# Performance work log

Measured on AMD Instinct MI355X. Metric: run time of the kernel, lower is better.

## Reference

```python
import jax, jax.numpy as jnp
import numpy as np

B, S, D_MODEL = 2, 2048, 768
N_QK, D_QK = 16, 16
N_OV, D_OV = 256, 1
VKV = 16
ROT_DIM, ROT_BASE = 16, 10000.0
SCALE = D_QK ** 0.5  # attn_scale defaults to sqrt(d_qk_head)


def _rotary_sin_cos(n_ctx, rotary_dim, base):
    # TransformerLens-style, non-adjacent pairs (GPT-NeoX)
    pos = jnp.arange(n_ctx, dtype=jnp.float32)
    dim = jnp.arange(rotary_dim // 2, dtype=jnp.float32)
    freq = base ** (dim / (rotary_dim / 2))
    freq = jnp.concatenate([freq, freq])  # 'd -> (2 d)'
    angles = pos[:, None] / freq[None, :]  # [n_ctx, rotary_dim]
    return jnp.sin(angles), jnp.cos(angles)


def _apply_rotary(x, sin, cos):
    # x: [B, S, H, d_head]; rotate first ROT_DIM dims, pass through the rest
    s = x.shape[1]
    xr = x[..., :ROT_DIM]
    half = ROT_DIM // 2
    rot = jnp.concatenate([-xr[..., half:], xr[..., :half]], axis=-1)  # rotate_every_two (non-adjacent)
    xr = xr * cos[:s, None, :] + rot * sin[:s, None, :]
    return jnp.concatenate([xr, x[..., ROT_DIM:]], axis=-1) if x.shape[-1] > ROT_DIM else xr


def setup_inputs() -> dict:
    key = jax.random.key(0)
    ks = jax.random.split(key, 6)
    std_qk = np.sqrt(2.0 / (D_MODEL * D_QK))   # kaiming fan_in for [H, d_model, d_head]
    std_v = np.sqrt(2.0 / (D_MODEL * D_OV))
    std_o = np.sqrt(2.0 / (D_OV * D_MODEL))
    std_vk = np.sqrt(2.0 / (N_QK * D_QK))
    return {
        "resid": jax.random.normal(ks[0], (B, S, D_MODEL), jnp.float32),
        "W_Q": jax.random.normal(ks[1], (N_QK, D_MODEL, D_QK), jnp.float32) * std_qk,
        "W_K": jax.random.normal(ks[2], (N_QK, D_MODEL, D_QK), jnp.float32) * std_qk,
        "W_V": jax.random.normal(ks[3], (N_OV, D_MODEL, D_OV), jnp.float32) * std_v,
        "W_O": jax.random.normal(ks[4], (N_OV, D_OV, D_MODEL), jnp.float32) * std_o,
        "b_Q": jnp.zeros((N_QK, D_QK), jnp.float32),
        "b_K": jnp.zeros((N_QK, D_QK), jnp.float32),
        "b_V": jnp.zeros((N_OV, D_OV), jnp.float32),
        "b_O": jnp.zeros((D_MODEL,), jnp.float32),
        "virtual_k": jax.random.normal(ks[5], (VKV, N_QK, D_QK), jnp.float32) * std_vk,
        "virtual_v": jnp.zeros((VKV, N_OV, D_OV), jnp.float32),
    }


def reference(resid, W_Q, W_K, W_V, W_O, b_Q, b_K, b_V, b_O, virtual_k, virtual_v):
    b, s, _ = resid.shape
    sin, cos = _rotary_sin_cos(s, ROT_DIM, ROT_BASE)

    q = jnp.einsum('bsd,hde->bshe', resid, W_Q) + b_Q  # [B,S,N_QK,D_QK]
    k = jnp.einsum('bsd,hde->bshe', resid, W_K) + b_K
    v = jnp.einsum('bsd,hde->bshe', resid, W_V) + b_V  # [B,S,N_OV,1]

    q = _apply_rotary(q, sin, cos)
    k = _apply_rotary(k, sin, cos)

    # append virtual KV along key axis
    k = jnp.concatenate([k, jnp.broadcast_to(virtual_k[None], (b, VKV, N_QK, D_QK))], axis=1)
    v = jnp.concatenate([v, jnp.broadcast_to(virtual_v[None], (b, VKV, N_OV, D_OV))], axis=1)

    scores = jnp.einsum('bqhe,bkhe->bhqk', q, k) / SCALE  # [B,H,S,S+VKV]
    i = jnp.arange(s)[:, None]
    j = jnp.arange(s + VKV)[None, :]
    mask = (j - i) <= VKV  # tril(.., diagonal=VKV)
    scores = jnp.where(mask, scores, -jnp.inf)
    pattern = jax.nn.softmax(scores, axis=-1)
    pattern = jnp.where(jnp.isnan(pattern), 0.0, pattern)

    r = N_OV // N_QK
    v_r = v.transpose(0, 2, 1, 3).reshape(b, N_QK, r, s + VKV, D_OV)  # [B,n_qk,r,K,1]
    z = jnp.einsum('bnqk,bnrkh->bnrqh', pattern, v_r)  # [B,n_qk,r,S,1]
    z = z.reshape(b, N_OV, s, D_OV).transpose(0, 2, 1, 3)  # [B,S,N_OV,1]

    out = jnp.einsum('bqhd,hdm->bqm', z, W_O) + b_O  # [B,S,D_MODEL]
    return out
```

## Files before the change

### kernel.cpp

```cpp
#include <hip/hip_runtime.h>
#include <hip/hip_bf16.h>
#include <math.h>

#define B_   2
#define S_   2048
#define DM   768
#define H_   16
#define C_   256
#define VKV_ 16
#define SK   2064
#define SKP  2080
#define NT_  65

#define TSPLIT 16
#define MAXSP  5
#define NACT   164

typedef __attribute__((ext_vector_type(8))) short short8;
typedef __attribute__((ext_vector_type(4))) short short4v;
typedef __attribute__((ext_vector_type(4))) float f32x4;
typedef __attribute__((ext_vector_type(16))) float f32x16;
typedef __attribute__((ext_vector_type(4))) unsigned uint4v;

#define QSCALE 0.360673760222240851f
#define L2B8   1.6609640474436811f

__device__ __forceinline__ short tobf(float f) {
    union { float f; unsigned u; } x; x.f = f;
    unsigned r = x.u + 0x7FFFu + ((x.u >> 16) & 1u);
    return (short)(r >> 16);
}
__device__ __forceinline__ float frombf_lo(unsigned u) {
    union { unsigned u; float f; } x; x.u = u << 16; return x.f;
}
__device__ __forceinline__ float frombf_hi(unsigned u) {
    union { unsigned u; float f; } x; x.u = u & 0xFFFF0000u; return x.f;
}

__device__ __forceinline__ void gload_lds16(const short* g, short* l) {
    __builtin_amdgcn_global_load_lds(
        (const __attribute__((address_space(1))) unsigned int*)g,
        (__attribute__((address_space(3))) unsigned int*)l, 16, 0, 0);
}

#define NRES (4096*768/4)
#define NWQ  (768*768)
#define NWO  (768*256)
__global__ __launch_bounds__(256) void conv_all(
    const float* __restrict__ resid,
    const float* __restrict__ WQ, const float* __restrict__ WK,
    const float* __restrict__ WV, const float* __restrict__ WO,
    const float* __restrict__ bQ, const float* __restrict__ bK,
    const float* __restrict__ bV,
    const float* __restrict__ vKp, const float* __restrict__ vVp,
    short* __restrict__ Ab, short* __restrict__ Wqkv_t,
    short* __restrict__ WtO, float* __restrict__ bqkv,
    short* __restrict__ Kb2, short* __restrict__ Vt3)
{
    int t = blockIdx.x * 256 + threadIdx.x;
    if (t < NRES) {
        float4 v = *(const float4*)(resid + (size_t)t * 4);
        short4v o = { tobf(v.x), tobf(v.y), tobf(v.z), tobf(v.w) };
        *(short4v*)(Ab + (size_t)t * 4) = o;
        return;
    }
    t -= NRES;
    if (t < NWQ) {
        int cc, d;
        if (t < 512 * 768) {
            const int e    = t & 15;
            const int rest = t >> 4;
            d  = rest % 768;
            cc = (rest / 768) * 16 + e;
        } else { cc = t / 768; d = t % 768; }
        float w;
        if (cc < 256)      w = WQ[((size_t)(cc >> 4) * DM + d) * 16 + (cc & 15)];
        else if (cc < 512) w = WK[((size_t)((cc - 256) >> 4) * DM + d) * 16 + (cc & 15)];
        else               w = WV[(size_t)(cc - 512) * DM + d];
        Wqkv_t[(size_t)cc * 768 + d] = tobf(w);
        return;
    }
    t -= NWQ;
    if (t < NWO) {
        int c = t & 255, m = t >> 8;
        WtO[t] = tobf(WO[(size_t)c * DM + m]);
        return;
    }
    t -= NWO;
    if (t < 768) {
        bqkv[t] = (t < 256) ? bQ[t] : (t < 512 ? bK[t - 256] : bV[t - 512]);
        return;
    }
    t -= 768;
    if (t < 32 * 32) {
        const int bh = t >> 5;
        const int s  = S_ + (t & 31);
        const int h  = bh & 15;
        short kb[16], vb[16];
        if (s < SK) {
            const int tt = s - S_;
#pragma unroll
            for (int e = 0; e < 16; ++e) {
                kb[e] = tobf(vKp[(size_t)tt * 256 + h * 16 + e]);
                vb[e] = tobf(vVp[(size_t)tt * 256 + h * 16 + e]);
            }
        } else {
#pragma unroll
            for (int e = 0; e < 16; ++e) { kb[e] = 0; vb[e] = 0; }
        }
        const int t5 = s >> 5;
        short* kbase = Kb2 + ((size_t)bh * NT_ + t5) * 512 + (s & 31) * 8;
#pragma unroll
        for (int e = 0; e < 8; ++e)  { kbase[e] = kb[e]; kbase[256 + e] = kb[e + 8]; }
        short* vbase = Vt3 + ((size_t)bh * NT_ + t5) * 1024
                     + ((s >> 4) & 1) * 512 + ((s >> 3) & 1) * 8 + (s & 7);
#pragma unroll
        for (int dv = 0; dv < 16; ++dv) vbase[dv * 16] = vb[dv];
    }
}

__global__ __launch_bounds__(256) void mm_qkv(
    const short* __restrict__ A, const short* __restrict__ Bt,
    const float* __restrict__ bias,
    short* __restrict__ Qb2, short* __restrict__ Kb2, short* __restrict__ Vt3)
{
    __shared__ float CtS[64][65];
    short* As = (short*)&CtS[0][0];
    short* Bs = As + 4096;

    const int tid  = threadIdx.x;
    const int w    = tid >> 6;
    const int lane = tid & 63;
    const int wm   = w >> 1, wn = w & 1;
    const int g    = lane >> 4, c = lane & 15;

    const int linear = blockIdx.y * 12 + blockIdx.x;
    const int xcd  = linear & 7;
    const int jj2  = linear >> 3;
    const int m0   = (xcd * 8 + jj2 / 12) * 64;
    const int n0   = (jj2 % 12) * 64;

    f32x4 acc[2][2];
#pragma unroll
    for (int i = 0; i < 2; ++i)
#pragma unroll
        for (int j = 0; j < 2; ++j) acc[i][j] = (f32x4){0.f, 0.f, 0.f, 0.f};

    const int lr = lane >> 3;
    const int lc = lane & 7;

    for (int k0 = 0; k0 < 768; k0 += 64) {
#pragma unroll
        for (int i = 0; i < 2; ++i) {
            const int ch  = i * 4 + w;
            const int row = ch * 8 + lr;
            const int scc = lc ^ (row & 7);
            gload_lds16(A + (size_t)(m0 + row) * 768 + k0 + scc * 8, As + ch * 512);
        }
#pragma unroll
        for (int i = 0; i < 2; ++i) {
            const int ch  = i * 4 + w;
            const int row = ch * 8 + lr;
            const int scc = lc ^ (row & 7);
            gload_lds16(Bt + (size_t)(n0 + row) * 768 + k0 + scc * 8, Bs + ch * 512);
        }
        __syncthreads();
#pragma unroll
        for (int kk = 0; kk < 64; kk += 32) {
            short8 af[2], bf[2];
#pragma unroll
            for (int i = 0; i < 2; ++i) {
                const int row = wm * 32 + i * 16 + c;
                const int sc  = ((kk >> 3) + g) ^ (row & 7);
                af[i] = *(const short8*)(As + row * 64 + sc * 8);
            }
#pragma unroll
            for (int j = 0; j < 2; ++j) {
                const int row = wn * 32 + j * 16 + c;
                const int sc  = ((kk >> 3) + g) ^ (row & 7);
                bf[j] = *(const short8*)(Bs + row * 64 + sc * 8);
            }
#pragma unroll
            for (int i = 0; i < 2; ++i)
#pragma unroll
                for (int j = 0; j < 2; ++j)
                    acc[i][j] = __builtin_amdgcn_mfma_f32_16x16x32_bf16(
                        af[i], bf[j], acc[i][j], 0, 0, 0);
        }
        __syncthreads();
    }

#pragma unroll
    for (int i = 0; i < 2; ++i)
#pragma unroll
        for (int j = 0; j < 2; ++j)
#pragma unroll
            for (int r = 0; r < 4; ++r)
                CtS[wm * 32 + i * 16 + 4 * g + r][wn * 32 + j * 16 + c] = acc[i][j][r];
    __syncthreads();

    const int b = m0 >> 11;
    if (n0 < 512) {
        const int isQ   = n0 < 256;
        const int hbase = (n0 & 255) >> 4;
        const int srow = tid & 63;
        const int g16  = tid >> 6;
        const int s    = (m0 + srow) & 2047;
        const int bh   = b * 16 + hbase + g16;
        float v[16];
#pragma unroll
        for (int e = 0; e < 16; ++e)
            v[e] = CtS[srow][g16 * 16 + e] + bias[n0 + g16 * 16 + e];
        union { short s[16]; short8 v8[2]; } u;
#pragma unroll
        for (int e = 0; e < 8; ++e) {
            const float invf = __builtin_amdgcn_exp2f(-(float)e * L2B8);
            float sn, cs;
            __sincosf((float)s * invf, &sn, &cs);
            float o0 = v[e] * cs - v[e + 8] * sn;
            float o1 = v[e + 8] * cs + v[e] * sn;
            if (isQ) { o0 *= QSCALE; o1 *= QSCALE; }
            u.s[e] = tobf(o0); u.s[e + 8] = tobf(o1);
        }
        short* dst = (isQ ? Qb2 + ((size_t)bh * 64 + (s >> 5)) * 512
                          : Kb2 + ((size_t)bh * NT_ + (s >> 5)) * 512)
                   + (s & 31) * 8;
        *(short8*)dst         = u.v8[0];
        *(short8*)(dst + 256) = u.v8[1];
    } else {
        const int hbase = (n0 - 512) >> 4;
        const int dvl = tid & 63;
        const int rg  = tid >> 6;
        const int s0  = (m0 + rg * 16) & 2047;
        const int bh  = b * 16 + hbase + (dvl >> 4);
        const float bv = bias[n0 + dvl];
        union { short s[16]; short8 v8[2]; } u;
#pragma unroll
        for (int k = 0; k < 16; ++k)
            u.s[k] = tobf(CtS[rg * 16 + k][dvl] + bv);
        short* dst = Vt3 + ((size_t)bh * NT_ + (s0 >> 5)) * 1024
                   + ((s0 >> 4) & 1) * 512 + (dvl & 15) * 16;
        *(short8*)dst       = u.v8[0];
        *(short8*)(dst + 8) = u.v8[1];
    }
}

__global__ __launch_bounds__(256) void mm_out(
    const short* __restrict__ A, const short* __restrict__ Bt,
    const float* __restrict__ bias, float* __restrict__ Cout)
{
    __shared__ short As[4096];
    __shared__ short Bs[4096];

    const int tid  = threadIdx.x;
    const int w    = tid >> 6;
    const int lane = tid & 63;
    const int wm   = w >> 1, wn = w & 1;
    const int g    = lane >> 4, c = lane & 15;

    const int linear = blockIdx.y * 12 + blockIdx.x;
    const int xcd  = linear & 7;
    const int jj2  = linear >> 3;
    const int m0   = (xcd * 8 + jj2 / 12) * 64;
    const int n0   = (jj2 % 12) * 64;

    f32x4 acc[2][2];
#pragma unroll
    for (int i = 0; i < 2; ++i)
#pragma unroll
        for (int j = 0; j < 2; ++j) acc[i][j] = (f32x4){0.f, 0.f, 0.f, 0.f};

    const int lr = lane >> 3;
    const int lc = lane & 7;

    for (int k0 = 0; k0 < 256; k0 += 64) {
#pragma unroll
        for (int i = 0; i < 2; ++i) {
            const int ch  = i * 4 + w;
            const int row = ch * 8 + lr;
            const int scc = lc ^ (row & 7);
            gload_lds16(A + (size_t)(m0 + row) * 256 + k0 + scc * 8, As + ch * 512);
        }
#pragma unroll
        for (int i = 0; i < 2; ++i) {
            const int ch  = i * 4 + w;
            const int row = ch * 8 + lr;
            const int scc = lc ^ (row & 7);
            gload_lds16(Bt + (size_t)(n0 + row) * 256 + k0 + scc * 8, Bs + ch * 512);
        }
        __syncthreads();
#pragma unroll
        for (int kk = 0; kk < 64; kk += 32) {
            short8 af[2], bf[2];
#pragma unroll
            for (int i = 0; i < 2; ++i) {
                const int row = wm * 32 + i * 16 + c;
                const int sc  = ((kk >> 3) + g) ^ (row & 7);
                af[i] = *(const short8*)(As + row * 64 + sc * 8);
            }
#pragma unroll
            for (int j = 0; j < 2; ++j) {
                const int row = wn * 32 + j * 16 + c;
                const int sc  = ((kk >> 3) + g) ^ (row & 7);
                bf[j] = *(const short8*)(Bs + row * 64 + sc * 8);
            }
#pragma unroll
            for (int i = 0; i < 2; ++i)
#pragma unroll
                for (int j = 0; j < 2; ++j)
                    acc[i][j] = __builtin_amdgcn_mfma_f32_16x16x32_bf16(
                        af[i], bf[j], acc[i][j], 0, 0, 0);
        }
        __syncthreads();
    }
#pragma unroll
    for (int i = 0; i < 2; ++i)
#pragma unroll
        for (int j = 0; j < 2; ++j) {
            const int col = n0 + wn * 32 + j * 16 + c;
            const float bv = bias[col];
#pragma unroll
            for (int r = 0; r < 4; ++r) {
                const int row = m0 + wm * 32 + i * 16 + 4 * g + r;
                Cout[(size_t)row * DM + col] = acc[i][j][r] + bv;
            }
        }
}

__global__ __launch_bounds__(256) void attn_split(
    const short* __restrict__ Qb2, const short* __restrict__ Kb2,
    const short* __restrict__ Vt3, unsigned* __restrict__ PartA,
    float* __restrict__ PartL, short* __restrict__ Zb)
{
    const int w    = threadIdx.x >> 6;
    const int lane = threadIdx.x & 63;
    const int blk  = blockIdx.x;
    const int xcd  = blk & 7;
    const int j    = blk >> 3;
    const int bhl  = j / 41;
    const int slot = j - bhl * 41;
    const int bh   = xcd * 4 + bhl;
    const int r    = slot * 4 + w;
    int qt, sp;
    if (r < 49)       { sp = 1; qt = 15 + r; }
    else if (r < 82)  { sp = 2; qt = 31 + (r - 49); }
    else if (r < 99)  { sp = 3; qt = 47 + (r - 82); }
    else if (r == 99) { sp = 4; qt = 63; }
    else              { sp = 0; qt = 163 - r; }

    const int nt   = qt + 2;
    const int t0   = sp * TSPLIT;
    const int tend = min(t0 + TSPLIT, nt);

    const int hi = lane >> 5;
    const int qc = lane & 31;
    const int q0 = qt * 32;

    const f32x16 zero16 = {0,0,0,0,0,0,0,0,0,0,0,0,0,0,0,0};

    short8 qf = *(const short8*)(Qb2 + ((size_t)bh * 64 + qt) * 512 + lane * 8);

    f32x16 acc = zero16;
    float lsum = 0.f;

    const short* kbase = Kb2 + (size_t)bh * NT_ * 512 + lane * 8;
    const short* vbase = Vt3 + (size_t)bh * NT_ * 1024 + (lane & 15) * 16 + hi * 8;
    const int qv16  = q0 + qc + 16;
    const int tmask = (q0 + 17) >> 5;

#define LK(tt)  (*(const short8*)(kbase + (size_t)(tt) * 512))
#define LVA(tt) (*(const short8*)(vbase + (size_t)(tt) * 1024))
#define LVB(tt) (*(const short8*)(vbase + (size_t)(tt) * 1024 + 512))

#define SOFTMAX_TILE(S, tt, B1, B2)                                          \
    {                                                                        \
        if ((tt) >= tmask) {                                                 \
            const int kt_ = (tt) * 32;                                       \
            _Pragma("unroll")                                                \
            for (int rr = 0; rr < 16; ++rr) {                                \
                const int key = kt_ + (rr & 3) + 8 * (rr >> 2) + 4 * hi;     \
                S[rr] = (key <= qv16) ? S[rr] : -INFINITY;                   \
            }                                                                \
        }                                                                    \
        unsigned pk[8];                                                      \
        _Pragma("unroll")                                                    \
        for (int jj = 0; jj < 8; ++jj) {                                     \
            const float p0 = __builtin_amdgcn_exp2f(S[2 * jj]);              \
            const float p1 = __builtin_amdgcn_exp2f(S[2 * jj + 1]);          \
            lsum += p0 + p1;                                                 \
            asm("v_cvt_pk_bf16_f32 %0, %1, %2" : "=v"(pk[jj]) : "v"(p0), "v"(p1)); \
        }                                                                    \
        unsigned a0 = pk[0], a2 = pk[2], a1 = pk[1], a3 = pk[3];             \
        unsigned a4 = pk[4], a6 = pk[6], a5 = pk[5], a7 = pk[7];             \
        asm("v_permlane32_swap_b32 %0, %1" : "+v"(a0), "+v"(a2));            \
        asm("v_permlane32_swap_b32 %0, %1" : "+v"(a1), "+v"(a3));            \
        asm("v_permlane32_swap_b32 %0, %1" : "+v"(a4), "+v"(a6));            \
        asm("v_permlane32_swap_b32 %0, %1" : "+v"(a5), "+v"(a7));            \
        B1.u[0] = a0; B1.u[1] = a1; B1.u[2] = a2; B1.u[3] = a3;              \
        B2.u[0] = a4; B2.u[1] = a5; B2.u[2] = a6; B2.u[3] = a7;              \
    }

    const int npair_end = t0 + ((tend - t0) & ~1);

    if (t0 < npair_end) {
        short8 kfA = LK(t0),     vaA = LVA(t0),     vvA = LVB(t0);
        short8 kfB = LK(t0 + 1), vaB = LVA(t0 + 1), vvB = LVB(t0 + 1);

        for (int t = t0; t < npair_end; t += 2) {
            short8 kfA_n = kfA, vaA_n = vaA, vvA_n = vvA;
            short8 kfB_n = kfB, vaB_n = vaB, vvB_n = vvB;
            if (t + 2 < npair_end) {
                kfA_n = LK(t + 2); vaA_n = LVA(t + 2); vvA_n = LVB(t + 2);
                kfB_n = LK(t + 3); vaB_n = LVA(t + 3); vvB_n = LVB(t + 3);
            }

            __builtin_amdgcn_s_setprio(1);
            f32x16 S0 = __builtin_amdgcn_mfma_f32_32x32x16_bf16(kfA, qf, zero16, 0, 0, 0);
            f32x16 S1 = __builtin_amdgcn_mfma_f32_32x32x16_bf16(kfB, qf, zero16, 0, 0, 0);
            __builtin_amdgcn_s_setprio(0);

            union { unsigned u[4]; short8 v; } b1A, b2A, b1B, b2B;
            SOFTMAX_TILE(S0, t,     b1A, b2A);
            SOFTMAX_TILE(S1, t + 1, b1B, b2B);

            __builtin_amdgcn_s_setprio(1);
            acc = __builtin_amdgcn_mfma_f32_32x32x16_bf16(vaA, b1A.v, acc, 0, 0, 0);
            acc = __builtin_amdgcn_mfma_f32_32x32x16_bf16(vvA, b2A.v, acc, 0, 0, 0);
            acc = __builtin_amdgcn_mfma_f32_32x32x16_bf16(vaB, b1B.v, acc, 0, 0, 0);
            acc = __builtin_amdgcn_mfma_f32_32x32x16_bf16(vvB, b2B.v, acc, 0, 0, 0);
            __builtin_amdgcn_s_setprio(0);

            kfA = kfA_n; vaA = vaA_n; vvA = vvA_n;
            kfB = kfB_n; vaB = vaB_n; vvB = vvB_n;
        }
    }
    if (npair_end < tend) {
        const int t = npair_end;
        short8 kf = LK(t), va = LVA(t), vv = LVB(t);
        f32x16 S0 = __builtin_amdgcn_mfma_f32_32x32x16_bf16(kf, qf, zero16, 0, 0, 0);
        union { unsigned u[4]; short8 v; } b1, b2;
        SOFTMAX_TILE(S0, t, b1, b2);
        acc = __builtin_amdgcn_mfma_f32_32x32x16_bf16(va, b1.v, acc, 0, 0, 0);
        acc = __builtin_amdgcn_mfma_f32_32x32x16_bf16(vv, b2.v, acc, 0, 0, 0);
    }

    lsum += __shfl_xor(lsum, 32);

    if (sp == 0 && qt <= 14) {
        const float inv = 1.f / lsum;
        const int b = bh >> 4, h = bh & 15;
        short* zp = Zb + ((size_t)(b * S_ + q0 + qc)) * C_ + h * 16;
        unsigned o01, o23, o45, o67;
        float a0 = acc[0] * inv, a1 = acc[1] * inv, a2 = acc[2] * inv, a3 = acc[3] * inv;
        float a4 = acc[4] * inv, a5 = acc[5] * inv, a6 = acc[6] * inv, a7 = acc[7] * inv;
        asm("v_cvt_pk_bf16_f32 %0, %1, %2" : "=v"(o01) : "v"(a0), "v"(a1));
        asm("v_cvt_pk_bf16_f32 %0, %1, %2" : "=v"(o23) : "v"(a2), "v"(a3));
        asm("v_cvt_pk_bf16_f32 %0, %1, %2" : "=v"(o45) : "v"(a4), "v"(a5));
        asm("v_cvt_pk_bf16_f32 %0, %1, %2" : "=v"(o67) : "v"(a6), "v"(a7));
        *(unsigned*)(zp + 4 * hi)         = o01;
        *(unsigned*)(zp + 4 * hi + 2)     = o23;
        *(unsigned*)(zp + 8 + 4 * hi)     = o45;
        *(unsigned*)(zp + 8 + 4 * hi + 2) = o67;
        return;
    }

    uint4v pa;
    asm("v_cvt_pk_bf16_f32 %0, %1, %2" : "=v"(pa.x) : "v"(acc[0]), "v"(acc[1]));
    asm("v_cvt_pk_bf16_f32 %0, %1, %2" : "=v"(pa.y) : "v"(acc[2]), "v"(acc[3]));
    asm("v_cvt_pk_bf16_f32 %0, %1, %2" : "=v"(pa.z) : "v"(acc[4]), "v"(acc[5]));
    asm("v_cvt_pk_bf16_f32 %0, %1, %2" : "=v"(pa.w) : "v"(acc[6]), "v"(acc[7]));

    const int pidx = (bh * 64 + qt) * MAXSP + sp;
    *(uint4v*)(PartA + ((size_t)pidx * 64 + lane) * 4) = pa;
    if (hi == 0) PartL[(size_t)pidx * 32 + qc] = lsum;
}

__global__ __launch_bounds__(256) void attn_combine(
    const unsigned* __restrict__ PartA, const float* __restrict__ PartL,
    short* __restrict__ Zb)
{
    const int w    = threadIdx.x >> 6;
    const int lane = threadIdx.x & 63;
    const int wid  = blockIdx.x * 4 + w;
    const int bh   = wid / 49;
    const int qt   = 15 + (wid - bh * 49);
    const int hi   = lane >> 5;
    const int qc   = lane & 31;
    const int ns   = (qt + 2 + TSPLIT - 1) / TSPLIT;

    float a[8];
#pragma unroll
    for (int rr = 0; rr < 8; ++rr) a[rr] = 0.f;
    float lsum = 0.f;

    const int pbase = (bh * 64 + qt) * MAXSP;
    for (int sp = 0; sp < ns; ++sp) {
        uint4v pa = *(const uint4v*)(PartA + ((size_t)(pbase + sp) * 64 + lane) * 4);
        a[0] += frombf_lo(pa.x); a[1] += frombf_hi(pa.x);
        a[2] += frombf_lo(pa.y); a[3] += frombf_hi(pa.y);
        a[4] += frombf_lo(pa.z); a[5] += frombf_hi(pa.z);
        a[6] += frombf_lo(pa.w); a[7] += frombf_hi(pa.w);
        lsum += PartL[(size_t)(pbase + sp) * 32 + qc];
    }
    const float inv = 1.f / lsum;

    const int b = bh >> 4, h = bh & 15;
    const int q0 = qt * 32;
    short* zp = Zb + ((size_t)(b * S_ + q0 + qc)) * C_ + h * 16;
    unsigned o01, o23, o45, o67;
    {
        float a0 = a[0] * inv, a1 = a[1] * inv, a2 = a[2] * inv, a3 = a[3] * inv;
        float a4 = a[4] * inv, a5 = a[5] * inv, a6 = a[6] * inv, a7 = a[7] * inv;
        asm("v_cvt_pk_bf16_f32 %0, %1, %2" : "=v"(o01) : "v"(a0), "v"(a1));
        asm("v_cvt_pk_bf16_f32 %0, %1, %2" : "=v"(o23) : "v"(a2), "v"(a3));
        asm("v_cvt_pk_bf16_f32 %0, %1, %2" : "=v"(o45) : "v"(a4), "v"(a5));
        asm("v_cvt_pk_bf16_f32 %0, %1, %2" : "=v"(o67) : "v"(a6), "v"(a7));
    }
    *(unsigned*)(zp + 4 * hi)         = o01;
    *(unsigned*)(zp + 4 * hi + 2)     = o23;
    *(unsigned*)(zp + 8 + 4 * hi)     = o45;
    *(unsigned*)(zp + 8 + 4 * hi + 2) = o67;
}

extern "C" void kernel_launch(void* const* d_in, const int* in_sizes, int n_in,
                              void* d_out, int out_size, void* d_ws, size_t ws_size,
                              hipStream_t stream)
{
    const float* resid = (const float*)d_in[0];
    const float* WQ = (const float*)d_in[1];
    const float* WK = (const float*)d_in[2];
    const float* WV = (const float*)d_in[3];
    const float* WO = (const float*)d_in[4];
    const float* bQ = (const float*)d_in[5];
    const float* bK = (const float*)d_in[6];
    const float* bV = (const float*)d_in[7];
    const float* bO = (const float*)d_in[8];
    const float* vK = (const float*)d_in[9];
    const float* vV = (const float*)d_in[10];
    float* out = (float*)d_out;
    float* ws  = (float*)d_ws;

    short* Zb   = (short*)ws;
    float* bqkv = ws + 3145728;
    short* Ab   = (short*)(ws + 3145728 + 768);
    short* Wqt  = Ab + 3145728;
    short* WtO  = Wqt + 589824;
    short* Qb2  = WtO + 196608;
    short* Kb2  = Qb2 + 1048576;
    short* Vt3  = Kb2 + 1064960;
    unsigned* PartA = (unsigned*)(Vt3 + 2129920);
    float*    PartL = (float*)(PartA + 2621440);

    const int conv_total = NRES + NWQ + NWO + 768 + 1024;
    conv_all<<<dim3((conv_total + 255) / 256), 256, 0, stream>>>(
        resid, WQ, WK, WV, WO, bQ, bK, bV, vK, vV,
        Ab, Wqt, WtO, bqkv, Kb2, Vt3);
    mm_qkv<<<dim3(12, 64), 256, 0, stream>>>(Ab, Wqt, bqkv, Qb2, Kb2, Vt3);
    attn_split<<<dim3(32 * NACT / 4), 256, 0, stream>>>(Qb2, Kb2, Vt3, PartA, PartL, Zb);
    attn_combine<<<dim3(392), 256, 0, stream>>>(PartA, PartL, Zb);
    mm_out<<<dim3(12, 64), 256, 0, stream>>>(Zb, WtO, bO, out);
}
```

Baseline: 55.47 us.

## Fuse split-K attention combine into one kernel via in-block LDS reduction

Replaces the split attention kernel plus separate combine kernel with one kernel. Each block now owns one (head, query tile) for tiles 15-63, and its four waves each handle a 17-tile slice of keys and reduce their partials through shared memory. Tiles 0-14 are done by one wave each. This drops a kernel launch and the global round-trip of bf16 partials. In exchange, waves with short or empty key ranges sit idle inside a block, load balance changes, and the XCD-aware block mapping is gone.

```diff
diff --git a/kernel.cpp b/kernel.cpp
--- a/kernel.cpp
+++ b/kernel.cpp
@@ -12,15 +12,12 @@
 #define SKP  2080
 #define NT_  65
 
-#define TSPLIT 16
-#define MAXSP  5
-#define NACT   164
+#define TSPLIT 17
 
 typedef __attribute__((ext_vector_type(8))) short short8;
 typedef __attribute__((ext_vector_type(4))) short short4v;
 typedef __attribute__((ext_vector_type(4))) float f32x4;
 typedef __attribute__((ext_vector_type(16))) float f32x16;
-typedef __attribute__((ext_vector_type(4))) unsigned uint4v;
 
 #define QSCALE 0.360673760222240851f
 #define L2B8   1.6609640474436811f
@@ -29,12 +26,6 @@
     union { float f; unsigned u; } x; x.f = f;
     unsigned r = x.u + 0x7FFFu + ((x.u >> 16) & 1u);
     return (short)(r >> 16);
-}
-__device__ __forceinline__ float frombf_lo(unsigned u) {
-    union { unsigned u; float f; } x; x.u = u << 16; return x.f;
-}
-__device__ __forceinline__ float frombf_hi(unsigned u) {
-    union { unsigned u; float f; } x; x.u = u & 0xFFFF0000u; return x.f;
 }
 
 __device__ __forceinline__ void gload_lds16(const short* g, short* l) {
@@ -327,30 +318,34 @@
         }
 }
 
-__global__ __launch_bounds__(256) void attn_split(
+__global__ __launch_bounds__(256) void attn_all(
     const short* __restrict__ Qb2, const short* __restrict__ Kb2,
-    const short* __restrict__ Vt3, unsigned* __restrict__ PartA,
-    float* __restrict__ PartL, short* __restrict__ Zb)
+    const short* __restrict__ Vt3, short* __restrict__ Zb)
 {
+    __shared__ float accS[4][64][9];
+    __shared__ float lsumS[4][64];
+
     const int w    = threadIdx.x >> 6;
     const int lane = threadIdx.x & 63;
     const int blk  = blockIdx.x;
-    const int xcd  = blk & 7;
-    const int j    = blk >> 3;
-    const int bhl  = j / 41;
-    const int slot = j - bhl * 41;
-    const int bh   = xcd * 4 + bhl;
-    const int r    = slot * 4 + w;
-    int qt, sp;
-    if (r < 49)       { sp = 1; qt = 15 + r; }
-    else if (r < 82)  { sp = 2; qt = 31 + (r - 49); }
-    else if (r < 99)  { sp = 3; qt = 47 + (r - 82); }
-    else if (r == 99) { sp = 4; qt = 63; }
-    else              { sp = 0; qt = 163 - r; }
-
-    const int nt   = qt + 2;
-    const int t0   = sp * TSPLIT;
-    const int tend = min(t0 + TSPLIT, nt);
+
+    int bh, qt, t0, tend;
+    bool multi;
+    if (blk < 32 * 49) {
+        multi = true;
+        bh = blk / 49;
+        qt = 63 - (blk % 49);
+        const int nt = qt + 2;
+        t0   = w * TSPLIT;
+        tend = min(t0 + TSPLIT, nt);
+    } else {
+        multi = false;
+        const int wid = (blk - 32 * 49) * 4 + w;
+        bh = wid / 15;
+        qt = wid % 15;
+        t0 = 0;
+        tend = qt + 2;
+    }
 
     const int hi = lane >> 5;
     const int qc = lane & 31;
@@ -400,7 +395,7 @@
         B2.u[0] = a4; B2.u[1] = a5; B2.u[2] = a6; B2.u[3] = a7;              \
     }
 
-    const int npair_end = t0 + ((tend - t0) & ~1);
+    const int npair_end = t0 + (((tend - t0) > 0 ? (tend - t0) : 0) & ~1);
 
     if (t0 < npair_end) {
         short8 kfA = LK(t0),     vaA = LVA(t0),     vvA = LVB(t0);
@@ -446,7 +441,7 @@
 
     lsum += __shfl_xor(lsum, 32);
 
-    if (sp == 0 && qt <= 14) {
+    if (!multi) {
         const float inv = 1.f / lsum;
         const int b = bh >> 4, h = bh & 15;
         short* zp = Zb + ((size_t)(b * S_ + q0 + qc)) * C_ + h * 16;
@@ -464,62 +459,37 @@
         return;
     }
 
-    uint4v pa;
-    asm("v_cvt_pk_bf16_f32 %0, %1, %2" : "=v"(pa.x) : "v"(acc[0]), "v"(acc[1]));
-    asm("v_cvt_pk_bf16_f32 %0, %1, %2" : "=v"(pa.y) : "v"(acc[2]), "v"(acc[3]));
-    asm("v_cvt_pk_bf16_f32 %0, %1, %2" : "=v"(pa.z) : "v"(acc[4]), "v"(acc[5]));
-    asm("v_cvt_pk_bf16_f32 %0, %1, %2" : "=v"(pa.w) : "v"(acc[6]), "v"(acc[7]));
-
-    const int pidx = (bh * 64 + qt) * MAXSP + sp;
-    *(uint4v*)(PartA + ((size_t)pidx * 64 + lane) * 4) = pa;
-    if (hi == 0) PartL[(size_t)pidx * 32 + qc] = lsum;
-}
-
-__global__ __launch_bounds__(256) void attn_combine(
-    const unsigned* __restrict__ PartA, const float* __restrict__ PartL,
-    short* __restrict__ Zb)
-{
-    const int w    = threadIdx.x >> 6;
-    const int lane = threadIdx.x & 63;
-    const int wid  = blockIdx.x * 4 + w;
-    const int bh   = wid / 49;
-    const int qt   = 15 + (wid - bh * 49);
-    const int hi   = lane >> 5;
-    const int qc   = lane & 31;
-    const int ns   = (qt + 2 + TSPLIT - 1) / TSPLIT;
-
-    float a[8];
-#pragma unroll
-    for (int rr = 0; rr < 8; ++rr) a[rr] = 0.f;
-    float lsum = 0.f;
-
-    const int pbase = (bh * 64 + qt) * MAXSP;
-    for (int sp = 0; sp < ns; ++sp) {
-        uint4v pa = *(const uint4v*)(PartA + ((size_t)(pbase + sp) * 64 + lane) * 4);
-        a[0] += frombf_lo(pa.x); a[1] += frombf_hi(pa.x);
-        a[2] += frombf_lo(pa.y); a[3] += frombf_hi(pa.y);
-        a[4] += frombf_lo(pa.z); a[5] += frombf_hi(pa.z);
-        a[6] += frombf_lo(pa.w); a[7] += frombf_hi(pa.w);
-        lsum += PartL[(size_t)(pbase + sp) * 32 + qc];
-    }
-    const float inv = 1.f / lsum;
-
-    const int b = bh >> 4, h = bh & 15;
-    const int q0 = qt * 32;
-    short* zp = Zb + ((size_t)(b * S_ + q0 + qc)) * C_ + h * 16;
-    unsigned o01, o23, o45, o67;
-    {
+#pragma unroll
+    for (int rr = 0; rr < 8; ++rr) accS[w][lane][rr] = acc[rr];
+    lsumS[w][lane] = lsum;
+    __syncthreads();
+
+    if (w == 0) {
+        float a[8];
+#pragma unroll
+        for (int rr = 0; rr < 8; ++rr) a[rr] = 0.f;
+        float L = 0.f;
+#pragma unroll
+        for (int ww = 0; ww < 4; ++ww) {
+            L += lsumS[ww][lane];
+#pragma unroll
+            for (int rr = 0; rr < 8; ++rr) a[rr] += accS[ww][lane][rr];
+        }
+        const float inv = 1.f / L;
+        const int b = bh >> 4, h = bh & 15;
+        short* zp = Zb + ((size_t)(b * S_ + q0 + qc)) * C_ + h * 16;
+        unsigned o01, o23, o45, o67;
         float a0 = a[0] * inv, a1 = a[1] * inv, a2 = a[2] * inv, a3 = a[3] * inv;
         float a4 = a[4] * inv, a5 = a[5] * inv, a6 = a[6] * inv, a7 = a[7] * inv;
         asm("v_cvt_pk_bf16_f32 %0, %1, %2" : "=v"(o01) : "v"(a0), "v"(a1));
         asm("v_cvt_pk_bf16_f32 %0, %1, %2" : "=v"(o23) : "v"(a2), "v"(a3));
         asm("v_cvt_pk_bf16_f32 %0, %1, %2" : "=v"(o45) : "v"(a4), "v"(a5));
         asm("v_cvt_pk_bf16_f32 %0, %1, %2" : "=v"(o67) : "v"(a6), "v"(a7));
-    }
-    *(unsigned*)(zp + 4 * hi)         = o01;
-    *(unsigned*)(zp + 4 * hi + 2)     = o23;
-    *(unsigned*)(zp + 8 + 4 * hi)     = o45;
-    *(unsigned*)(zp + 8 + 4 * hi + 2) = o67;
+        *(unsigned*)(zp + 4 * hi)         = o01;
+        *(unsigned*)(zp + 4 * hi + 2)     = o23;
+        *(unsigned*)(zp + 8 + 4 * hi)     = o45;
+        *(unsigned*)(zp + 8 + 4 * hi + 2) = o67;
+    }
 }
 
 extern "C" void kernel_launch(void* const* d_in, const int* in_sizes, int n_in,
@@ -548,15 +518,12 @@
     short* Qb2  = WtO + 196608;
     short* Kb2  = Qb2 + 1048576;
     short* Vt3  = Kb2 + 1064960;
-    unsigned* PartA = (unsigned*)(Vt3 + 2129920);
-    float*    PartL = (float*)(PartA + 2621440);
 
     const int conv_total = NRES + NWQ + NWO + 768 + 1024;
     conv_all<<<dim3((conv_total + 255) / 256), 256, 0, stream>>>(
         resid, WQ, WK, WV, WO, bQ, bK, bV, vK, vV,
         Ab, Wqt, WtO, bqkv, Kb2, Vt3);
     mm_qkv<<<dim3(12, 64), 256, 0, stream>>>(Ab, Wqt, bqkv, Qb2, Kb2, Vt3);
-    attn_split<<<dim3(32 * NACT / 4), 256, 0, stream>>>(Qb2, Kb2, Vt3, PartA, PartL, Zb);
-    attn_combine<<<dim3(392), 256, 0, stream>>>(PartA, PartL, Zb);
+    attn_all<<<dim3(32 * 49 + 120), 256, 0, stream>>>(Qb2, Kb2, Vt3, Zb);
     mm_out<<<dim3(12, 64), 256, 0, stream>>>(Zb, WtO, bO, out);
 }
```

Result: slower. 56.88 us, median of 2 (+2.5%).
